# Kernel tuning notes

Hardware: AMD Instinct MI355X
Metric: run time of the kernel (lower is better)

## Reference

```python
import jax, jax.numpy as jnp
import numpy as np

D_MODEL = 2048
N_HEADS = 16
HEAD_DIM = D_MODEL // N_HEADS
ROPE_BASE = 10000.0


def rope(x):
    # x: [b, h, s, d]; matches the torch module exactly:
    # x1 = even dims, x2 = odd dims; output = concat([x1*cos - x2*sin, x1*sin + x2*cos], -1)
    b, h, s, d = x.shape
    theta = 1.0 / ROPE_BASE ** (jnp.arange(0, d, 2, dtype=jnp.float32) / d)  # [d/2]
    angles = jnp.arange(s, dtype=jnp.float32)[:, None] * theta[None, :]       # [s, d/2]
    cos = jnp.cos(angles)[None, None]  # [1,1,s,d/2]
    sin = jnp.sin(angles)[None, None]
    x1, x2 = x[..., ::2], x[..., 1::2]
    return jnp.concatenate([x1 * cos - x2 * sin, x1 * sin + x2 * cos], axis=-1)


def setup_inputs() -> dict:
    key = jax.random.key(0)
    ks = jax.random.split(key, 5)
    b, s = 2, 2048
    x = jax.random.normal(ks[0], (b, s, D_MODEL), dtype=jnp.float32)
    scale_in = 1.0 / np.sqrt(D_MODEL)
    Wqkv = jax.random.normal(ks[1], (D_MODEL, 3 * D_MODEL), dtype=jnp.float32) * scale_in
    bqkv = jnp.zeros((3 * D_MODEL,), dtype=jnp.float32)
    Wo = jax.random.normal(ks[2], (D_MODEL, D_MODEL), dtype=jnp.float32) * scale_in
    bo = jnp.zeros((D_MODEL,), dtype=jnp.float32)
    return {"x": x, "Wqkv": Wqkv, "bqkv": bqkv, "Wo": Wo, "bo": bo}


def reference(x, Wqkv, bqkv, Wo, bo):
    b, s, d = x.shape
    qkv = x @ Wqkv + bqkv                      # [b, s, 3d]
    q, k, v = jnp.split(qkv, 3, axis=-1)
    def to_heads(t):
        return t.reshape(b, s, N_HEADS, HEAD_DIM).transpose(0, 2, 1, 3)  # [b,h,s,hd]
    q, k, v = to_heads(q), to_heads(k), to_heads(v)
    q = rope(q)
    k = rope(k)
    scores = jnp.einsum('bhqd,bhkd->bhqk', q, k) / jnp.sqrt(jnp.float32(HEAD_DIM))
    attn = jax.nn.softmax(scores, axis=-1)
    out = jnp.einsum('bhqk,bhkd->bhqd', attn, v)
    out = out.transpose(0, 2, 1, 3).reshape(b, s, d)
    return out @ Wo + bo
```

## Files before the change

kernel.cpp:

```cpp
#include <hip/hip_runtime.h>
#include <hip/hip_bf16.h>
#include <cstdint>
#include <type_traits>

#define D_MODEL 2048
#define NH 16
#define HD 128
#define SEQ 2048
#define QKV_LD (3 * D_MODEL)

typedef __attribute__((ext_vector_type(8))) short short8;
typedef __attribute__((ext_vector_type(4))) float f32x4;
typedef __attribute__((ext_vector_type(16))) float f32x16;

__device__ __forceinline__ ushort f2bf(float f) {
    union { float f; uint32_t u; } c; c.f = f;
    uint32_t u = c.u;
    uint32_t r = (u + 0x7FFFu + ((u >> 16) & 1u)) >> 16;
    return (ushort)r;
}
__device__ __forceinline__ float bf2f(ushort b) {
    union { uint32_t u; float f; } c; c.u = ((uint32_t)b) << 16;
    return c.f;
}

__device__ __forceinline__ void load_lds16(const ushort* g, ushort* l) {
    __builtin_amdgcn_global_load_lds(
        (const __attribute__((address_space(1))) void*)g,
        (__attribute__((address_space(3))) void*)l, 16, 0, 0);
}

__global__ void cvt_bf16_kernel(const float* __restrict__ in, ushort* __restrict__ out, int n4) {
    int idx = blockIdx.x * blockDim.x + threadIdx.x;
    if (idx >= n4) return;
    float4 v = ((const float4*)in)[idx];
    ushort4 o;
    o.x = f2bf(v.x); o.y = f2bf(v.y); o.z = f2bf(v.z); o.w = f2bf(v.w);
    ((ushort4*)out)[idx] = o;
}

__global__ void transpose_bf16_kernel(const float* __restrict__ in, ushort* __restrict__ out,
                                      int R, int C) {
    __shared__ float tile[32][33];
    int tx = threadIdx.x, ty = threadIdx.y;
    int c0 = blockIdx.x * 32, r0 = blockIdx.y * 32;
    for (int i = 0; i < 4; ++i) {
        int r = r0 + ty + i * 8;
        tile[ty + i * 8][tx] = in[(size_t)r * C + c0 + tx];
    }
    __syncthreads();
    for (int i = 0; i < 4; ++i) {
        int c = c0 + ty + i * 8;
        out[(size_t)c * R + r0 + tx] = f2bf(tile[tx][ty + i * 8]);
    }
}

#define STAGE_A(L, T_, B_) load_lds16(Ag + (size_t)(L) * 64 * K + (size_t)(T_) * 64, \
                                      smA + (B_) * 16384 + (L) * 4096 + ldsW)
#define STAGE_B(L, T_, B_) load_lds16(Bg + (size_t)(L) * 64 * K + (size_t)(T_) * 64, \
                                      smB + (B_) * 16384 + (L) * 4096 + ldsW)
#define READ_A(MH) do { const ushort* _ab = smA + cb * 16384 + aRow + (MH) * 4096; \
    _Pragma("unroll") for (int i_ = 0; i_ < 4; ++i_) { \
        af[i_][0] = *(const short8*)(_ab + i_ * 1024 + pc0); \
        af[i_][1] = *(const short8*)(_ab + i_ * 1024 + pc1); } } while (0)
#define READ_B(NHh) do { const ushort* _bb = smB + cb * 16384 + bRow + (NHh) * 2048; \
    _Pragma("unroll") for (int j_ = 0; j_ < 2; ++j_) { \
        bfr[j_][0] = *(const short8*)(_bb + j_ * 1024 + pc0); \
        bfr[j_][1] = *(const short8*)(_bb + j_ * 1024 + pc1); } } while (0)
#define MFMA16(MH, NHh) do { \
    _Pragma("unroll") for (int i_ = 0; i_ < 4; ++i_) \
    _Pragma("unroll") for (int j_ = 0; j_ < 2; ++j_) { \
        acc[(MH) * 4 + i_][(NHh) * 2 + j_] = __builtin_amdgcn_mfma_f32_16x16x32_bf16( \
            af[i_][0], bfr[j_][0], acc[(MH) * 4 + i_][(NHh) * 2 + j_], 0, 0, 0); \
        acc[(MH) * 4 + i_][(NHh) * 2 + j_] = __builtin_amdgcn_mfma_f32_16x16x32_bf16( \
            af[i_][1], bfr[j_][1], acc[(MH) * 4 + i_][(NHh) * 2 + j_], 0, 0, 0); } } while (0)

template <typename OutT>
__global__ __launch_bounds__(512, 2) void gemm256(
    const ushort* __restrict__ A,
    const ushort* __restrict__ Bt,
    const float* __restrict__ bias,
    OutT* __restrict__ C,
    int M, int N, int K)
{
    __shared__ __align__(16) ushort sm[65536];
    ushort* smA = sm;
    ushort* smB = sm + 32768;

    int t = threadIdx.x;
    int w = t >> 6, lane = t & 63;
    int lr = lane & 15, lh = lane >> 4;
    int wm_idx = w >> 2, wn_idx = w & 3;
    int m0 = blockIdx.y * 256, n0 = blockIdx.x * 256;

    int srow = t >> 3;
    int scol = ((t & 7) ^ (srow & 7)) << 3;
    const ushort* Ag = A + (size_t)(m0 + srow) * K + scol;
    const ushort* Bg = Bt + (size_t)(n0 + srow) * K + scol;
    int ldsW = w * 512;

    int pc0 = (lh ^ (lr & 7)) << 3;
    int pc1 = ((4 + lh) ^ (lr & 7)) << 3;
    int aRow = (wm_idx * 128 + lr) * 64;
    int bRow = (wn_idx * 64 + lr) * 64;

    f32x4 acc[8][4];
#pragma unroll
    for (int i = 0; i < 8; ++i)
#pragma unroll
        for (int j = 0; j < 4; ++j) acc[i][j] = (f32x4)0.0f;
    short8 af[4][2], bfr[2][2];

    int NT = K >> 6;

    STAGE_A(0, 0, 0); STAGE_A(1, 0, 0); STAGE_A(2, 0, 0); STAGE_A(3, 0, 0);
    STAGE_B(0, 0, 0); STAGE_B(1, 0, 0); STAGE_B(2, 0, 0); STAGE_B(3, 0, 0);
    if (NT > 1) {
        STAGE_A(0, 1, 1); STAGE_A(2, 1, 1);
        asm volatile("s_waitcnt vmcnt(2)" ::: "memory");
    } else {
        asm volatile("s_waitcnt vmcnt(0)" ::: "memory");
    }
    __builtin_amdgcn_s_barrier();
    __builtin_amdgcn_sched_barrier(0);

    for (int T = 0; T < NT; ++T) {
        int cb = T & 1, nb = cb ^ 1;
        READ_A(0); READ_B(0);
        if (T + 1 < NT) { STAGE_A(1, T + 1, nb); STAGE_A(3, T + 1, nb); }
        __builtin_amdgcn_s_barrier();
        __builtin_amdgcn_s_setprio(1); MFMA16(0, 0); __builtin_amdgcn_s_setprio(0);
        __builtin_amdgcn_s_barrier();
        READ_B(1);
        if (T + 1 < NT) { STAGE_B(0, T + 1, nb); STAGE_B(1, T + 1, nb); }
        __builtin_amdgcn_s_barrier();
        __builtin_amdgcn_s_setprio(1); MFMA16(0, 1); __builtin_amdgcn_s_setprio(0);
        __builtin_amdgcn_s_barrier();
        READ_A(1); READ_B(0);
        if (T + 1 < NT) { STAGE_B(2, T + 1, nb); STAGE_B(3, T + 1, nb); }
        if (T + 2 < NT) { STAGE_A(0, T + 2, cb); STAGE_A(2, T + 2, cb); }
        __builtin_amdgcn_s_barrier();
        __builtin_amdgcn_s_setprio(1); MFMA16(1, 0); __builtin_amdgcn_s_setprio(0);
        __builtin_amdgcn_s_barrier();
        READ_B(1);
        __builtin_amdgcn_s_barrier();
        __builtin_amdgcn_s_setprio(1); MFMA16(1, 1); __builtin_amdgcn_s_setprio(0);
        if (T + 2 < NT) asm volatile("s_waitcnt vmcnt(2)" ::: "memory");
        else            asm volatile("s_waitcnt vmcnt(0)" ::: "memory");
        __builtin_amdgcn_s_barrier();
        __builtin_amdgcn_sched_barrier(0);
    }

    float bv[4];
#pragma unroll
    for (int jj = 0; jj < 4; ++jj) bv[jj] = bias[n0 + wn_idx * 64 + jj * 16 + lr];
#pragma unroll
    for (int ii = 0; ii < 8; ++ii) {
        int row = m0 + wm_idx * 128 + ii * 16 + lh * 4;
#pragma unroll
        for (int jj = 0; jj < 4; ++jj) {
            int col = n0 + wn_idx * 64 + jj * 16 + lr;
#pragma unroll
            for (int r = 0; r < 4; ++r) {
                float v = acc[ii][jj][r] + bv[jj];
                if constexpr (std::is_same<OutT, ushort>::value)
                    C[(size_t)(row + r) * N + col] = f2bf(v);
                else
                    C[(size_t)(row + r) * N + col] = v;
            }
        }
    }
}

__global__ void rope_table(float2* __restrict__ tab) {
    int i = blockIdx.x * blockDim.x + threadIdx.x;
    int s = i >> 6, j = i & 63;
    float theta = powf(10000.0f, -(float)j * (1.0f / 64.0f));
    float ang = (float)s * theta;
    float sn, cs;
    sincosf(ang, &sn, &cs);
    tab[i] = make_float2(cs, sn);
}

__global__ void rope_cast_qk(const ushort* __restrict__ qkv,
                             const float2* __restrict__ tab,
                             ushort* __restrict__ Qb, ushort* __restrict__ Kb) {
    int t = threadIdx.x;
    int wv = blockIdx.x * 4 + (t >> 6);
    int j = t & 63;
    int bs = wv >> 5;
    int rem = wv & 31;
    int which = rem >> 4;
    int h = rem & 15;
    int s = bs & 2047;
    int b = bs >> 11;
    size_t src = (size_t)bs * QKV_LD + which * D_MODEL + h * HD;
    uint32_t pr = *(const uint32_t*)(qkv + src + 2 * j);
    float x1 = bf2f((ushort)(pr & 0xffff));
    float x2 = bf2f((ushort)(pr >> 16));
    float2 cspair = tab[(s << 6) + j];
    float cs = cspair.x, sn = cspair.y;
    float sc = which ? 1.0f : 0.08838834764831845f;
    float o1 = (x1 * cs - x2 * sn) * sc;
    float o2 = (x1 * sn + x2 * cs) * sc;
    ushort* dst = which ? Kb : Qb;
    size_t obase = ((size_t)(b * NH + h) * SEQ + s) * HD;
    dst[obase + j] = f2bf(o1);
    dst[obase + 64 + j] = f2bf(o2);
}

__global__ void v_transpose(const ushort* __restrict__ qkv, ushort* __restrict__ Vt) {
    __shared__ ushort tile[32][33];
    int tx = threadIdx.x, ty = threadIdx.y;
    int s0 = blockIdx.x * 32;
    int d0 = blockIdx.y * 32;
    int bh = blockIdx.z;
    int b = bh >> 4, h = bh & 15;
    for (int i = 0; i < 4; ++i) {
        int s = s0 + ty + i * 8;
        tile[ty + i * 8][tx] = qkv[((size_t)(b * SEQ + s)) * QKV_LD + 2 * D_MODEL + h * HD + d0 + tx];
    }
    __syncthreads();
    for (int i = 0; i < 4; ++i) {
        int d = d0 + ty + i * 8;
        Vt[((size_t)bh * HD + d) * SEQ + s0 + tx] = tile[tx][ty + i * 8];
    }
}

__global__ __launch_bounds__(256) void attn_mfma(const ushort* __restrict__ Qb,
                                                 const ushort* __restrict__ Kb,
                                                 const ushort* __restrict__ Vt,
                                                 ushort* __restrict__ ctx) {
    __shared__ ushort smem[25600];
    ushort* Ks = smem;
    ushort* Vts = smem + 8192;
    ushort* Ps = smem + 16384;

    int t = threadIdx.x;
    int w = t >> 6, l = t & 63;
    int l31 = l & 31, g = l >> 5;
    int q0 = blockIdx.x * 128;
    int bh = blockIdx.y;
    int b = bh >> 4, h = bh & 15;

    int qrow = q0 + w * 32 + l31;
    const ushort* Qg = Qb + ((size_t)bh * SEQ + qrow) * HD;
    short8 qf[8];
#pragma unroll
    for (int kc = 0; kc < 8; kc++)
        qf[kc] = *(const short8*)(Qg + kc * 16 + g * 8);

    f32x16 O[4];
#pragma unroll
    for (int di = 0; di < 4; di++) O[di] = (f32x16)0.0f;
    float m_run = -INFINITY, l_run = 0.0f;

    const ushort* KgB = Kb + (size_t)bh * SEQ * HD;
    const ushort* VtB = Vt + (size_t)bh * HD * SEQ;

    for (int k0 = 0; k0 < SEQ; k0 += 64) {
        __syncthreads();
#pragma unroll
        for (int c2 = 0; c2 < 4; c2++) {
            int f = c2 * 256 + t;
            int r = f >> 4, c = f & 15;
            int cp = c ^ (r & 15);
            uint4 v = *(const uint4*)(KgB + (size_t)(k0 + r) * HD + c * 8);
            *(uint4*)(Ks + r * 128 + cp * 8) = v;
        }
#pragma unroll
        for (int c2 = 0; c2 < 4; c2++) {
            int f = c2 * 256 + t;
            int d = f >> 3, c = f & 7;
            int cp = c ^ (d & 7);
            uint4 v = *(const uint4*)(VtB + (size_t)d * SEQ + k0 + c * 8);
            *(uint4*)(Vts + d * 64 + cp * 8) = v;
        }
        __syncthreads();

        f32x16 St[2];
        St[0] = (f32x16)0.0f;
        St[1] = (f32x16)0.0f;
#pragma unroll
        for (int ki = 0; ki < 2; ki++) {
            int row = ki * 32 + l31;
#pragma unroll
            for (int kc = 0; kc < 8; kc++) {
                int cp = (kc * 2 + g) ^ (row & 15);
                short8 a = *(const short8*)(Ks + row * 128 + cp * 8);
                St[ki] = __builtin_amdgcn_mfma_f32_32x32x16_bf16(a, qf[kc], St[ki], 0, 0, 0);
            }
        }

        float mx = -INFINITY;
#pragma unroll
        for (int ki = 0; ki < 2; ki++)
#pragma unroll
            for (int r = 0; r < 16; r++) mx = fmaxf(mx, St[ki][r]);
        mx = fmaxf(mx, __shfl_xor(mx, 32));
        float mn = fmaxf(m_run, mx);
        float alpha = __expf(m_run - mn);
        m_run = mn;
        float psum = 0.0f;
#pragma unroll
        for (int ki = 0; ki < 2; ki++)
#pragma unroll
            for (int r = 0; r < 16; r++) {
                float p = __expf(St[ki][r] - mn);
                St[ki][r] = p;
                psum += p;
            }
        psum += __shfl_xor(psum, 32);
        l_run = l_run * alpha + psum;
#pragma unroll
        for (int di = 0; di < 4; di++)
#pragma unroll
            for (int r = 0; r < 16; r++) O[di][r] *= alpha;

        {
            int qloc = w * 32 + l31;
            ushort* Pr = Ps + qloc * 72;
#pragma unroll
            for (int ki = 0; ki < 2; ki++)
#pragma unroll
                for (int u = 0; u < 4; u++) {
                    ushort4 pk;
                    pk.x = f2bf(St[ki][4 * u + 0]);
                    pk.y = f2bf(St[ki][4 * u + 1]);
                    pk.z = f2bf(St[ki][4 * u + 2]);
                    pk.w = f2bf(St[ki][4 * u + 3]);
                    *(ushort4*)(Pr + ki * 32 + 8 * u + 4 * g) = pk;
                }
        }

        {
            int qloc = w * 32 + l31;
            short8 pb[4];
#pragma unroll
            for (int kc = 0; kc < 4; kc++)
                pb[kc] = *(const short8*)(Ps + qloc * 72 + kc * 16 + g * 8);
#pragma unroll
            for (int di = 0; di < 4; di++) {
                int d = di * 32 + l31;
#pragma unroll
                for (int kc = 0; kc < 4; kc++) {
                    int cp = (kc * 2 + g) ^ (d & 7);
                    short8 va = *(const short8*)(Vts + d * 64 + cp * 8);
                    O[di] = __builtin_amdgcn_mfma_f32_32x32x16_bf16(va, pb[kc], O[di], 0, 0, 0);
                }
            }
        }
    }

    __syncthreads();
    float inv = 1.0f / l_run;
    ushort* ob = smem;
    {
        int qloc = w * 32 + l31;
        ushort* orow = ob + qloc * 128;
#pragma unroll
        for (int di = 0; di < 4; di++)
#pragma unroll
            for (int u = 0; u < 4; u++) {
                ushort4 pk;
                pk.x = f2bf(O[di][4 * u + 0] * inv);
                pk.y = f2bf(O[di][4 * u + 1] * inv);
                pk.z = f2bf(O[di][4 * u + 2] * inv);
                pk.w = f2bf(O[di][4 * u + 3] * inv);
                *(ushort4*)(orow + di * 32 + 8 * u + 4 * g) = pk;
            }
    }
#pragma unroll
    for (int p = 0; p < 8; p++) {
        int qloc = w * 32 + p * 4 + (l >> 4);
        int c16 = l & 15;
        uint4 v = *(const uint4*)(ob + qloc * 128 + c16 * 8);
        size_t tok = (size_t)b * SEQ + q0 + qloc;
        *(uint4*)(ctx + tok * D_MODEL + h * HD + c16 * 8) = v;
    }
}

extern "C" void kernel_launch(void* const* d_in, const int* in_sizes, int n_in,
                              void* d_out, int out_size, void* d_ws, size_t ws_size,
                              hipStream_t stream) {
    const float* x    = (const float*)d_in[0];
    const float* Wqkv = (const float*)d_in[1];
    const float* bqkv = (const float*)d_in[2];
    const float* Wo   = (const float*)d_in[3];
    const float* bo   = (const float*)d_in[4];
    float* out = (float*)d_out;

    char* ws = (char*)d_ws;
    ushort* x_bf   = (ushort*)(ws);
    ushort* wqkvT  = (ushort*)(ws + 16777216);
    ushort* woT    = (ushort*)(ws + 41943040);
    ushort* qkv_bf = (ushort*)(ws + 50331648);
    ushort* Qb     = (ushort*)(ws + 100663296);
    ushort* Kb     = (ushort*)(ws + 117440512);
    ushort* VtG    = (ushort*)(ws + 134217728);
    ushort* ctx    = (ushort*)(ws + 150994944);
    float2* rtab   = (float2*)(ws + 150994944);

    rope_table<<<512, 256, 0, stream>>>(rtab);
    cvt_bf16_kernel<<<8192, 256, 0, stream>>>(x, x_bf, 2097152);
    transpose_bf16_kernel<<<dim3(192, 64), dim3(32, 8), 0, stream>>>(Wqkv, wqkvT, 2048, 6144);
    transpose_bf16_kernel<<<dim3(64, 64), dim3(32, 8), 0, stream>>>(Wo, woT, 2048, 2048);
    gemm256<ushort><<<dim3(24, 16), 512, 0, stream>>>(x_bf, wqkvT, bqkv, qkv_bf, 4096, 6144, 2048);
    rope_cast_qk<<<32768, 256, 0, stream>>>(qkv_bf, rtab, Qb, Kb);
    v_transpose<<<dim3(64, 4, 32), dim3(32, 8), 0, stream>>>(qkv_bf, VtG);
    attn_mfma<<<dim3(16, 32), 256, 0, stream>>>(Qb, Kb, VtG, ctx);
    gemm256<float><<<dim3(8, 16), 512, 0, stream>>>(ctx, woT, bo, out, 4096, 2048, 2048);
}
```

Baseline: 450.5 us.

## Restructure GEMM LDS staging order and B-tile row mapping with explicit waits

Reorders the B-tile global-to-LDS mapping so each N-half occupies a contiguous LDS region, and reschedules the double-buffered prefetch so all next-tile loads are issued within the current iteration rather than two tiles ahead. It adds explicit vmcnt/lgkmcnt waits and sched barriers around each MFMA phase and reorders the MFMA quadrants so B fragments are reused. The aim is tighter control of load/compute overlap and fewer LDS hazards, at the cost of more barriers and possibly less prefetch distance.

```diff
diff --git a/kernel.cpp b/kernel.cpp
--- a/kernel.cpp
+++ b/kernel.cpp
@@ -55,15 +55,21 @@
     }
 }
 
+#define WAITV(N) asm volatile("s_waitcnt vmcnt(" #N ")" ::: "memory")
+#define LGKM0()  do { asm volatile("s_waitcnt lgkmcnt(0)" ::: "memory"); \
+                      __builtin_amdgcn_sched_barrier(0); } while (0)
+#define BAR()    do { __builtin_amdgcn_s_barrier(); \
+                      __builtin_amdgcn_sched_barrier(0); } while (0)
+
 #define STAGE_A(L, T_, B_) load_lds16(Ag + (size_t)(L) * 64 * K + (size_t)(T_) * 64, \
                                       smA + (B_) * 16384 + (L) * 4096 + ldsW)
-#define STAGE_B(L, T_, B_) load_lds16(Bg + (size_t)(L) * 64 * K + (size_t)(T_) * 64, \
+#define STAGE_B(L, T_, B_) load_lds16(Bg + (size_t)(((L) & 1) * 128 + ((L) >> 1) * 32) * K + (size_t)(T_) * 64, \
                                       smB + (B_) * 16384 + (L) * 4096 + ldsW)
 #define READ_A(MH) do { const ushort* _ab = smA + cb * 16384 + aRow + (MH) * 4096; \
     _Pragma("unroll") for (int i_ = 0; i_ < 4; ++i_) { \
         af[i_][0] = *(const short8*)(_ab + i_ * 1024 + pc0); \
         af[i_][1] = *(const short8*)(_ab + i_ * 1024 + pc1); } } while (0)
-#define READ_B(NHh) do { const ushort* _bb = smB + cb * 16384 + bRow + (NHh) * 2048; \
+#define READ_B(NHh) do { const ushort* _bb = smB + cb * 16384 + (NHh) * 8192 + bRow; \
     _Pragma("unroll") for (int j_ = 0; j_ < 2; ++j_) { \
         bfr[j_][0] = *(const short8*)(_bb + j_ * 1024 + pc0); \
         bfr[j_][1] = *(const short8*)(_bb + j_ * 1024 + pc1); } } while (0)
@@ -96,13 +102,14 @@
     int srow = t >> 3;
     int scol = ((t & 7) ^ (srow & 7)) << 3;
     const ushort* Ag = A + (size_t)(m0 + srow) * K + scol;
-    const ushort* Bg = Bt + (size_t)(n0 + srow) * K + scol;
+    int bq = (srow >> 5) * 64 + (srow & 31);
+    const ushort* Bg = Bt + (size_t)(n0 + bq) * K + scol;
     int ldsW = w * 512;
 
     int pc0 = (lh ^ (lr & 7)) << 3;
     int pc1 = ((4 + lh) ^ (lr & 7)) << 3;
     int aRow = (wm_idx * 128 + lr) * 64;
-    int bRow = (wn_idx * 64 + lr) * 64;
+    int bRow = (wn_idx * 32 + lr) * 64;
 
     f32x4 acc[8][4];
 #pragma unroll
@@ -113,42 +120,38 @@
 
     int NT = K >> 6;
 
-    STAGE_A(0, 0, 0); STAGE_A(1, 0, 0); STAGE_A(2, 0, 0); STAGE_A(3, 0, 0);
-    STAGE_B(0, 0, 0); STAGE_B(1, 0, 0); STAGE_B(2, 0, 0); STAGE_B(3, 0, 0);
-    if (NT > 1) {
-        STAGE_A(0, 1, 1); STAGE_A(2, 1, 1);
-        asm volatile("s_waitcnt vmcnt(2)" ::: "memory");
-    } else {
-        asm volatile("s_waitcnt vmcnt(0)" ::: "memory");
-    }
-    __builtin_amdgcn_s_barrier();
-    __builtin_amdgcn_sched_barrier(0);
+    STAGE_A(0, 0, 0); STAGE_A(2, 0, 0); STAGE_B(0, 0, 0); STAGE_B(1, 0, 0);
+    STAGE_B(2, 0, 0); STAGE_B(3, 0, 0);
+    STAGE_A(1, 0, 0); STAGE_A(3, 0, 0);
+    WAITV(4);
+    BAR();
 
     for (int T = 0; T < NT; ++T) {
         int cb = T & 1, nb = cb ^ 1;
+        bool pf = (T + 1 < NT);
         READ_A(0); READ_B(0);
-        if (T + 1 < NT) { STAGE_A(1, T + 1, nb); STAGE_A(3, T + 1, nb); }
-        __builtin_amdgcn_s_barrier();
+        if (pf) { STAGE_A(0, T + 1, nb); STAGE_A(2, T + 1, nb);
+                  STAGE_B(0, T + 1, nb); STAGE_B(1, T + 1, nb); }
+        BAR(); LGKM0();
         __builtin_amdgcn_s_setprio(1); MFMA16(0, 0); __builtin_amdgcn_s_setprio(0);
-        __builtin_amdgcn_s_barrier();
+        if (pf) WAITV(6); else WAITV(2);
+        BAR();
         READ_B(1);
-        if (T + 1 < NT) { STAGE_B(0, T + 1, nb); STAGE_B(1, T + 1, nb); }
-        __builtin_amdgcn_s_barrier();
+        if (pf) { STAGE_B(2, T + 1, nb); STAGE_B(3, T + 1, nb); }
+        BAR(); LGKM0();
         __builtin_amdgcn_s_setprio(1); MFMA16(0, 1); __builtin_amdgcn_s_setprio(0);
-        __builtin_amdgcn_s_barrier();
-        READ_A(1); READ_B(0);
-        if (T + 1 < NT) { STAGE_B(2, T + 1, nb); STAGE_B(3, T + 1, nb); }
-        if (T + 2 < NT) { STAGE_A(0, T + 2, cb); STAGE_A(2, T + 2, cb); }
-        __builtin_amdgcn_s_barrier();
+        if (pf) WAITV(6); else WAITV(0);
+        BAR();
+        READ_A(1);
+        if (pf) { STAGE_A(1, T + 1, nb); STAGE_A(3, T + 1, nb); }
+        BAR(); LGKM0();
+        __builtin_amdgcn_s_setprio(1); MFMA16(1, 1); __builtin_amdgcn_s_setprio(0);
+        BAR();
+        READ_B(0);
+        BAR(); LGKM0();
         __builtin_amdgcn_s_setprio(1); MFMA16(1, 0); __builtin_amdgcn_s_setprio(0);
-        __builtin_amdgcn_s_barrier();
-        READ_B(1);
-        __builtin_amdgcn_s_barrier();
-        __builtin_amdgcn_s_setprio(1); MFMA16(1, 1); __builtin_amdgcn_s_setprio(0);
-        if (T + 2 < NT) asm volatile("s_waitcnt vmcnt(2)" ::: "memory");
-        else            asm volatile("s_waitcnt vmcnt(0)" ::: "memory");
-        __builtin_amdgcn_s_barrier();
-        __builtin_amdgcn_sched_barrier(0);
+        WAITV(4);
+        BAR();
     }
 
     float bv[4];
```

Result: no change. 447.2 us (-0.7%).
